# Performance work log

Measured on AMD Instinct MI355X. Metric: run time of the kernel, lower is better.

Reference implementation:

```python
import jax, jax.numpy as jnp
import numpy as np

THRESHOLD = 0.004  # graph_threshold from init_kwargs
EPS = 1e-12


def setup_inputs() -> dict:
    key = jax.random.key(0)
    kf, kw = jax.random.split(key)
    features = jax.random.normal(kf, (8192, 128), dtype=jnp.float32)
    weight = jax.random.normal(kw, (128, 128), dtype=jnp.float32)
    return {"features": features, "weight": weight}


def reference(features, weight):
    # Pairwise state fidelity: squared dot product of row-normalized vectors.
    n = features.shape[0]
    xn = features / (jnp.linalg.norm(features, axis=1, keepdims=True) + EPS)
    fid = (xn @ xn.T) ** 2  # [N, N]
    # Edge weight 1.0 where fid >= threshold (secondary=None); no self-loops.
    adj = (fid >= THRESHOLD).astype(features.dtype)
    adj = adj * (1.0 - jnp.eye(n, dtype=features.dtype))
    aggregated = adj @ features  # [N, F]
    # relu(W @ agg.T).T == relu(agg @ W.T)
    return jax.nn.relu(aggregated @ weight.T)
```

## Files before the change

### kernel.cpp

```cpp
#include <hip/hip_runtime.h>
#include <math.h>

#define NROWS 8192
#define NF    128
#define THRF  0.004f
#define BM    128
#define BN    64
#define QN    2048
#define NITER 32

typedef _Float16 f16;
typedef __attribute__((ext_vector_type(8))) _Float16 f16x8;
typedef __attribute__((ext_vector_type(4))) float f32x4;

#define MFMA16F(a, b, c) __builtin_amdgcn_mfma_f32_16x16x32_f16(a, b, c, 0, 0, 0)

#define RH_OFF 0
#define RL_OFF 32768
#define TB_OFF 65536
#define PB_OFF 98304
#define IJ_OFF 114688
#define SM_BYTES 115200

typedef __attribute__((address_space(1))) const unsigned int g_u32;
typedef __attribute__((address_space(3))) unsigned int l_u32;

__device__ __forceinline__ void gload16(const void* g, void* l) {
    __builtin_amdgcn_global_load_lds((g_u32*)g, (l_u32*)l, 16, 0, 0);
}

__device__ __forceinline__ unsigned short f16bits(f16 x) {
    return __builtin_bit_cast(unsigned short, x);
}

__global__ __launch_bounds__(256) void zero_k(float* __restrict__ out) {
    int idx = blockIdx.x * 512 + threadIdx.x;
    f32x4 z = {0.f, 0.f, 0.f, 0.f};
    reinterpret_cast<f32x4*>(out)[idx]       = z;
    reinterpret_cast<f32x4*>(out)[idx + 256] = z;
}

__global__ __launch_bounds__(256) void prep_k(const float* __restrict__ X,
                                              float* __restrict__ inv_norm,
                                              unsigned short* __restrict__ Xh,
                                              unsigned short* __restrict__ Xl,
                                              unsigned short* __restrict__ XhT) {
    __shared__ unsigned short sT[64][136];
    const int t  = threadIdx.x;
    const int jb = blockIdx.x * 64;
    const int row = t >> 2, c0 = (t & 3) * 32;
    const int grow = jb + row;

    float v[32];
    {
        const float* src = X + (size_t)grow * NF + c0;
        #pragma unroll
        for (int k = 0; k < 8; ++k) {
            f32x4 e = *reinterpret_cast<const f32x4*>(src + 4 * k);
            v[4 * k]     = e[0]; v[4 * k + 1] = e[1];
            v[4 * k + 2] = e[2]; v[4 * k + 3] = e[3];
        }
    }
    float ss = 0.f;
    #pragma unroll
    for (int k = 0; k < 32; ++k) ss += v[k] * v[k];
    ss += __shfl_xor(ss, 1);
    ss += __shfl_xor(ss, 2);
    if ((t & 3) == 0) inv_norm[grow] = 1.0f / (sqrtf(ss) + 1e-12f);

    #pragma unroll
    for (int k = 0; k < 4; ++k) {
        unsigned hw[4], lw[4];
        #pragma unroll
        for (int p = 0; p < 4; ++p) {
            float a = v[8 * k + 2 * p], b = v[8 * k + 2 * p + 1];
            f16 ha = (f16)a, hb = (f16)b;
            f16 la = (f16)((a - (float)ha) * 2048.0f);
            f16 lb = (f16)((b - (float)hb) * 2048.0f);
            hw[p] = (unsigned)f16bits(ha) | ((unsigned)f16bits(hb) << 16);
            lw[p] = (unsigned)f16bits(la) | ((unsigned)f16bits(lb) << 16);
        }
        uint4 h4 = {hw[0], hw[1], hw[2], hw[3]};
        uint4 l4 = {lw[0], lw[1], lw[2], lw[3]};
        *reinterpret_cast<uint4*>(Xh + (size_t)grow * NF + c0 + 8 * k) = h4;
        *reinterpret_cast<uint4*>(Xl + (size_t)grow * NF + c0 + 8 * k) = l4;
        unsigned* sp = reinterpret_cast<unsigned*>(&sT[row][c0 + 8 * k]);
        sp[0] = hw[0]; sp[1] = hw[1]; sp[2] = hw[2]; sp[3] = hw[3];
    }
    __syncthreads();
    {
        int f = t >> 1, qh = t & 1;
        unsigned um[16];
        #pragma unroll
        for (int m = 0; m < 16; ++m) {
            int j = 32 * qh + 2 * m;
            um[m] = (unsigned)sT[j][f] | ((unsigned)sT[j + 1][f] << 16);
        }
        unsigned* dst = reinterpret_cast<unsigned*>(XhT + (size_t)f * NROWS + jb + 32 * qh);
        #pragma unroll
        for (int m = 0; m < 16; ++m) dst[m] = um[m];
    }
}

__device__ __forceinline__ void issue_tiles(const unsigned short* __restrict__ Xh,
                                            const unsigned short* __restrict__ Xl,
                                            const unsigned short* __restrict__ XhT,
                                            char* SM, int w, int l, int jwin, int buf) {
    const int r16 = l >> 4, c16 = l & 15;
    #pragma unroll
    for (int u = 0; u < 2; ++u) {
        int jloc = 8 * w + 4 * u + r16;
        size_t src = (size_t)(jwin + jloc) * NF + ((c16 ^ (jloc & 15)) << 3);
        gload16(Xh + src, SM + RH_OFF + buf * 16384 + (8 * w + 4 * u) * 256);
        gload16(Xl + src, SM + RL_OFF + buf * 16384 + (8 * w + 4 * u) * 256);
    }
    const int r8 = l >> 3, c8 = l & 7;
    #pragma unroll
    for (int u = 0; u < 2; ++u) {
        int floc = 16 * w + 8 * u + r8;
        const unsigned short* src = XhT + (size_t)floc * NROWS + jwin + ((c8 ^ (floc & 7)) << 3);
        gload16(src, SM + TB_OFF + buf * 16384 + (16 * w + 8 * u) * 128);
    }
}

__global__ __launch_bounds__(512, 2) void fused_k(const unsigned short* __restrict__ Xh,
                                                  const unsigned short* __restrict__ Xl,
                                                  const unsigned short* __restrict__ XhT,
                                                  const float* __restrict__ inv_norm,
                                                  float* __restrict__ out) {
    __shared__ __align__(16) char SM[SM_BYTES];
    const int t = threadIdx.x;
    const int w = t >> 6, l = t & 63, l15 = l & 15, h = l >> 4;
    const int im2 = w >> 1;
    const int jn2 = w & 1;
    const int bid   = blockIdx.x;
    const int ibase = (bid >> 2) * BM;
    const int qbase = (bid & 3) * QN;

    f16x8 aH[2][4], aL[2][4];
    #pragma unroll
    for (int is = 0; is < 2; ++is) {
        const size_t ro = (size_t)(ibase + 32 * im2 + 16 * is + l15) * NF;
        #pragma unroll
        for (int ks = 0; ks < 4; ++ks) {
            aH[is][ks] = *reinterpret_cast<const f16x8*>(Xh + ro + 32 * ks + 8 * h);
            aL[is][ks] = *reinterpret_cast<const f16x8*>(Xl + ro + 32 * ks + 8 * h);
        }
    }
    float invI2[8];
    #pragma unroll
    for (int is = 0; is < 2; ++is)
        #pragma unroll
        for (int q = 0; q < 4; ++q) {
            float x = inv_norm[ibase + 32 * im2 + 16 * is + 4 * h + q];
            invI2[is * 4 + q] = x * x;
        }

    issue_tiles(Xh, Xl, XhT, SM, w, l, qbase, 0);
    if (t < BN) { float x = inv_norm[qbase + t]; ((float*)(SM + IJ_OFF))[t] = x * x; }

    f32x4 agg[2][4];
    #pragma unroll
    for (int is = 0; is < 2; ++is)
        #pragma unroll
        for (int fs = 0; fs < 4; ++fs)
            #pragma unroll
            for (int q = 0; q < 4; ++q) agg[is][fs][q] = 0.f;

    for (int it = 0; it < NITER; ++it) {
        const int buf  = it & 1;
        const int jwin = qbase + it * BN;
        __syncthreads();
        if (it + 1 < NITER) {
            issue_tiles(Xh, Xl, XhT, SM, w, l, jwin + BN, buf ^ 1);
            if (t < BN) {
                float x = inv_norm[jwin + BN + t];
                ((float*)(SM + IJ_OFF))[(buf ^ 1) * BN + t] = x * x;
            }
        }
        const char* rh = SM + RH_OFF + buf * 16384;
        const char* rl = SM + RL_OFF + buf * 16384;
        f32x4 Shi[2][2], Slo[2][2];
        #pragma unroll
        for (int js = 0; js < 2; ++js)
            #pragma unroll
            for (int is = 0; is < 2; ++is)
                #pragma unroll
                for (int q = 0; q < 4; ++q) { Shi[js][is][q] = 0.f; Slo[js][is][q] = 0.f; }
        __builtin_amdgcn_s_setprio(1);
        #pragma unroll
        for (int ks = 0; ks < 4; ++ks) {
            #pragma unroll
            for (int js = 0; js < 2; ++js) {
                int jl = 32 * jn2 + 16 * js + l15;
                int boff = jl * 256 + (((4 * ks + h) ^ (jl & 15)) << 4);
                f16x8 bh = *reinterpret_cast<const f16x8*>(rh + boff);
                f16x8 bl = *reinterpret_cast<const f16x8*>(rl + boff);
                #pragma unroll
                for (int is = 0; is < 2; ++is) {
                    Shi[js][is] = MFMA16F(aH[is][ks], bh, Shi[js][is]);
                    Slo[js][is] = MFMA16F(aL[is][ks], bh, Slo[js][is]);
                    Slo[js][is] = MFMA16F(aH[is][ks], bl, Slo[js][is]);
                }
            }
        }
        __builtin_amdgcn_s_setprio(0);

        #pragma unroll
        for (int js = 0; js < 2; ++js) {
            int jc = 32 * jn2 + 16 * js + l15;
            float ij2 = ((const float*)(SM + IJ_OFF))[buf * BN + jc];
            #pragma unroll
            for (int is = 0; is < 2; ++is) {
                int di = (jwin + jc) - (ibase + 32 * im2 + 16 * is + 4 * h);
                #pragma unroll
                for (int q = 0; q < 4; ++q) {
                    float vv = Shi[js][is][q] + Slo[js][is][q] * (1.0f / 2048.0f);
                    float t2 = vv * vv * invI2[is * 4 + q] * ij2;
                    bool p = (t2 >= THRF) && (di != q);
                    int il = 32 * im2 + 16 * is + 4 * h + q;
                    int pb = il * 128 + ((jc * 2) ^ ((il & 7) << 4));
                    *reinterpret_cast<unsigned short*>(SM + PB_OFF + pb) =
                        p ? (unsigned short)0x3C00 : (unsigned short)0;
                }
            }
        }
        asm volatile("s_waitcnt lgkmcnt(0)\n\ts_barrier" ::: "memory");

        const char* tbp = SM + TB_OFF + buf * 16384;
        __builtin_amdgcn_s_setprio(1);
        #pragma unroll
        for (int kj = 0; kj < 2; ++kj) {
            f16x8 pa[2];
            #pragma unroll
            for (int is = 0; is < 2; ++is) {
                int ir = 32 * im2 + 16 * is + l15;
                pa[is] = *reinterpret_cast<const f16x8*>(
                    SM + PB_OFF + ir * 128 + ((64 * kj + 16 * h) ^ ((ir & 7) << 4)));
            }
            #pragma unroll
            for (int fs = 0; fs < 4; ++fs) {
                int f = 64 * jn2 + 16 * fs + l15;
                f16x8 bt = *reinterpret_cast<const f16x8*>(
                    tbp + f * 128 + ((64 * kj + 16 * h) ^ ((f & 7) << 4)));
                agg[0][fs] = MFMA16F(pa[0], bt, agg[0][fs]);
                agg[1][fs] = MFMA16F(pa[1], bt, agg[1][fs]);
            }
        }
        __builtin_amdgcn_s_setprio(0);
    }

    #pragma unroll
    for (int is = 0; is < 2; ++is)
        #pragma unroll
        for (int fs = 0; fs < 4; ++fs) {
            int col = 64 * jn2 + 16 * fs + l15;
            #pragma unroll
            for (int q = 0; q < 4; ++q) {
                int row = ibase + 32 * im2 + 16 * is + 4 * h + q;
                atomicAdd(&out[(size_t)row * NF + col], agg[is][fs][q]);
            }
        }
}

__global__ __launch_bounds__(256) void combine_k(const float* __restrict__ Wm,
                                                 float* __restrict__ out) {
    __shared__ float sW[NF * NF];
    __shared__ float sSum[32][132];
    const int t = threadIdx.x;
    const size_t base = (size_t)blockIdx.x * 32 * NF;
    #pragma unroll
    for (int k = 0; k < 16; ++k) {
        int u4 = t + 256 * k;
        reinterpret_cast<f32x4*>(sW)[u4] = reinterpret_cast<const f32x4*>(Wm)[u4];
    }
    #pragma unroll
    for (int k = 0; k < 4; ++k) {
        int u4 = t + 256 * k;
        f32x4 v = reinterpret_cast<const f32x4*>(out + base)[u4];
        *reinterpret_cast<f32x4*>(&sSum[u4 >> 5][(4 * u4) & 127]) = v;
    }
    __syncthreads();
    const int r = t & 31, og = t >> 5;
    float acc[16];
    #pragma unroll
    for (int oi = 0; oi < 16; ++oi) acc[oi] = 0.f;
    #pragma unroll 8
    for (int k4 = 0; k4 < 32; ++k4) {
        f32x4 a4 = *reinterpret_cast<const f32x4*>(&sSum[r][4 * k4]);
        #pragma unroll
        for (int oi = 0; oi < 16; ++oi) {
            f32x4 w4 = *reinterpret_cast<const f32x4*>(&sW[(og * 16 + oi) * NF + 4 * k4]);
            acc[oi] += a4[0] * w4[0] + a4[1] * w4[1] + a4[2] * w4[2] + a4[3] * w4[3];
        }
    }
    #pragma unroll
    for (int o4 = 0; o4 < 4; ++o4) {
        f32x4 v4;
        #pragma unroll
        for (int e = 0; e < 4; ++e) {
            float v = acc[o4 * 4 + e];
            v4[e] = v > 0.f ? v : 0.f;
        }
        *reinterpret_cast<f32x4*>(out + base + r * NF + og * 16 + o4 * 4) = v4;
    }
}

extern "C" void kernel_launch(void* const* d_in, const int* in_sizes, int n_in,
                              void* d_out, int out_size, void* d_ws, size_t ws_size,
                              hipStream_t stream) {
    const float* feat = (const float*)d_in[0];
    const float* Wm   = (const float*)d_in[1];
    float* out        = (float*)d_out;

    char* ws = (char*)d_ws;
    unsigned short* Xh  = (unsigned short*)(ws);
    unsigned short* Xl  = (unsigned short*)(ws + (2u << 20));
    unsigned short* XhT = (unsigned short*)(ws + (4u << 20));
    float* inv_norm     = (float*)(ws + (6u << 20));

    zero_k<<<NROWS * NF / 2048, 256, 0, stream>>>(out);
    prep_k<<<NROWS / 64, 256, 0, stream>>>(feat, inv_norm, Xh, Xl, XhT);
    fused_k<<<256, 512, 0, stream>>>(Xh, Xl, XhT, inv_norm, out);
    combine_k<<<NROWS / 32, 256, 0, stream>>>(Wm, out);
}
```

Before: 107.6 us.

## Split fused kernel into dedicated producer and consumer wavefronts

Adds four producer wavefronts per block (768 threads) that issue all global-to-LDS tile loads and inverse-norm staging, while the original eight wavefronts only run the MFMA fidelity and aggregation stages. This takes load-issue work off the compute waves so prefetch overlaps compute more cleanly. The cost is extra threads per block, a launch bound change that may restrict registers per thread, and producers that sit idle at every barrier. Each block still needs about 115 KB of LDS, so the requested three blocks per CU likely cannot co-reside.

```diff
diff --git a/kernel.cpp b/kernel.cpp
--- a/kernel.cpp
+++ b/kernel.cpp
@@ -102,28 +102,28 @@
     }
 }
 
-__device__ __forceinline__ void issue_tiles(const unsigned short* __restrict__ Xh,
-                                            const unsigned short* __restrict__ Xl,
-                                            const unsigned short* __restrict__ XhT,
-                                            char* SM, int w, int l, int jwin, int buf) {
+__device__ __forceinline__ void issue_tiles_p(const unsigned short* __restrict__ Xh,
+                                              const unsigned short* __restrict__ Xl,
+                                              const unsigned short* __restrict__ XhT,
+                                              char* SM, int p, int l, int jwin, int buf) {
     const int r16 = l >> 4, c16 = l & 15;
     #pragma unroll
-    for (int u = 0; u < 2; ++u) {
-        int jloc = 8 * w + 4 * u + r16;
+    for (int u = 0; u < 4; ++u) {
+        int jloc = 16 * p + 4 * u + r16;
         size_t src = (size_t)(jwin + jloc) * NF + ((c16 ^ (jloc & 15)) << 3);
-        gload16(Xh + src, SM + RH_OFF + buf * 16384 + (8 * w + 4 * u) * 256);
-        gload16(Xl + src, SM + RL_OFF + buf * 16384 + (8 * w + 4 * u) * 256);
+        gload16(Xh + src, SM + RH_OFF + buf * 16384 + (16 * p + 4 * u) * 256);
+        gload16(Xl + src, SM + RL_OFF + buf * 16384 + (16 * p + 4 * u) * 256);
     }
     const int r8 = l >> 3, c8 = l & 7;
     #pragma unroll
-    for (int u = 0; u < 2; ++u) {
-        int floc = 16 * w + 8 * u + r8;
+    for (int u = 0; u < 4; ++u) {
+        int floc = 32 * p + 8 * u + r8;
         const unsigned short* src = XhT + (size_t)floc * NROWS + jwin + ((c8 ^ (floc & 7)) << 3);
-        gload16(src, SM + TB_OFF + buf * 16384 + (16 * w + 8 * u) * 128);
-    }
-}
-
-__global__ __launch_bounds__(512, 2) void fused_k(const unsigned short* __restrict__ Xh,
+        gload16(src, SM + TB_OFF + buf * 16384 + (32 * p + 8 * u) * 128);
+    }
+}
+
+__global__ __launch_bounds__(768, 3) void fused_k(const unsigned short* __restrict__ Xh,
                                                   const unsigned short* __restrict__ Xl,
                                                   const unsigned short* __restrict__ XhT,
                                                   const float* __restrict__ inv_norm,
@@ -131,33 +131,46 @@
     __shared__ __align__(16) char SM[SM_BYTES];
     const int t = threadIdx.x;
     const int w = t >> 6, l = t & 63, l15 = l & 15, h = l >> 4;
-    const int im2 = w >> 1;
+    const bool producer = (w >= 8);
+    const int im2 = (w >> 1) & 3;
     const int jn2 = w & 1;
     const int bid   = blockIdx.x;
     const int ibase = (bid >> 2) * BM;
     const int qbase = (bid & 3) * QN;
 
     f16x8 aH[2][4], aL[2][4];
-    #pragma unroll
-    for (int is = 0; is < 2; ++is) {
-        const size_t ro = (size_t)(ibase + 32 * im2 + 16 * is + l15) * NF;
-        #pragma unroll
-        for (int ks = 0; ks < 4; ++ks) {
-            aH[is][ks] = *reinterpret_cast<const f16x8*>(Xh + ro + 32 * ks + 8 * h);
-            aL[is][ks] = *reinterpret_cast<const f16x8*>(Xl + ro + 32 * ks + 8 * h);
-        }
-    }
     float invI2[8];
-    #pragma unroll
-    for (int is = 0; is < 2; ++is)
-        #pragma unroll
-        for (int q = 0; q < 4; ++q) {
-            float x = inv_norm[ibase + 32 * im2 + 16 * is + 4 * h + q];
-            invI2[is * 4 + q] = x * x;
-        }
-
-    issue_tiles(Xh, Xl, XhT, SM, w, l, qbase, 0);
-    if (t < BN) { float x = inv_norm[qbase + t]; ((float*)(SM + IJ_OFF))[t] = x * x; }
+    if (!producer) {
+        #pragma unroll
+        for (int is = 0; is < 2; ++is) {
+            const size_t ro = (size_t)(ibase + 32 * im2 + 16 * is + l15) * NF;
+            #pragma unroll
+            for (int ks = 0; ks < 4; ++ks) {
+                aH[is][ks] = *reinterpret_cast<const f16x8*>(Xh + ro + 32 * ks + 8 * h);
+                aL[is][ks] = *reinterpret_cast<const f16x8*>(Xl + ro + 32 * ks + 8 * h);
+            }
+        }
+        #pragma unroll
+        for (int is = 0; is < 2; ++is)
+            #pragma unroll
+            for (int ks = 0; ks < 4; ++ks) {
+                asm volatile("" : "+v"(aH[is][ks]));
+                asm volatile("" : "+v"(aL[is][ks]));
+            }
+        #pragma unroll
+        for (int is = 0; is < 2; ++is)
+            #pragma unroll
+            for (int q = 0; q < 4; ++q) {
+                float x = inv_norm[ibase + 32 * im2 + 16 * is + 4 * h + q];
+                invI2[is * 4 + q] = x * x;
+            }
+    } else {
+        issue_tiles_p(Xh, Xl, XhT, SM, w - 8, l, qbase, 0);
+        if (w == 8) {
+            float x = inv_norm[qbase + l];
+            ((float*)(SM + IJ_OFF))[l] = x * x;
+        }
+    }
 
     f32x4 agg[2][4];
     #pragma unroll
@@ -171,96 +184,103 @@
         const int buf  = it & 1;
         const int jwin = qbase + it * BN;
         __syncthreads();
-        if (it + 1 < NITER) {
-            issue_tiles(Xh, Xl, XhT, SM, w, l, jwin + BN, buf ^ 1);
-            if (t < BN) {
-                float x = inv_norm[jwin + BN + t];
-                ((float*)(SM + IJ_OFF))[(buf ^ 1) * BN + t] = x * x;
-            }
-        }
-        const char* rh = SM + RH_OFF + buf * 16384;
-        const char* rl = SM + RL_OFF + buf * 16384;
-        f32x4 Shi[2][2], Slo[2][2];
-        #pragma unroll
-        for (int js = 0; js < 2; ++js)
-            #pragma unroll
-            for (int is = 0; is < 2; ++is)
-                #pragma unroll
-                for (int q = 0; q < 4; ++q) { Shi[js][is][q] = 0.f; Slo[js][is][q] = 0.f; }
-        __builtin_amdgcn_s_setprio(1);
-        #pragma unroll
-        for (int ks = 0; ks < 4; ++ks) {
+        if (producer) {
+            if (it + 1 < NITER) {
+                issue_tiles_p(Xh, Xl, XhT, SM, w - 8, l, jwin + BN, buf ^ 1);
+                if (w == 8) {
+                    float x = inv_norm[jwin + BN + l];
+                    ((float*)(SM + IJ_OFF))[(buf ^ 1) * BN + l] = x * x;
+                }
+            }
+        } else {
+            const char* rh = SM + RH_OFF + buf * 16384;
+            const char* rl = SM + RL_OFF + buf * 16384;
+            f32x4 Shi[2][2], Slo[2][2];
+            #pragma unroll
+            for (int js = 0; js < 2; ++js)
+                #pragma unroll
+                for (int is = 0; is < 2; ++is)
+                    #pragma unroll
+                    for (int q = 0; q < 4; ++q) { Shi[js][is][q] = 0.f; Slo[js][is][q] = 0.f; }
+            __builtin_amdgcn_s_setprio(1);
+            #pragma unroll
+            for (int ks = 0; ks < 4; ++ks) {
+                #pragma unroll
+                for (int js = 0; js < 2; ++js) {
+                    int jl = 32 * jn2 + 16 * js + l15;
+                    int boff = jl * 256 + (((4 * ks + h) ^ (jl & 15)) << 4);
+                    f16x8 bh = *reinterpret_cast<const f16x8*>(rh + boff);
+                    f16x8 bl = *reinterpret_cast<const f16x8*>(rl + boff);
+                    #pragma unroll
+                    for (int is = 0; is < 2; ++is) {
+                        Shi[js][is] = MFMA16F(aH[is][ks], bh, Shi[js][is]);
+                        Slo[js][is] = MFMA16F(aL[is][ks], bh, Slo[js][is]);
+                        Slo[js][is] = MFMA16F(aH[is][ks], bl, Slo[js][is]);
+                    }
+                }
+            }
+            __builtin_amdgcn_s_setprio(0);
+
             #pragma unroll
             for (int js = 0; js < 2; ++js) {
-                int jl = 32 * jn2 + 16 * js + l15;
-                int boff = jl * 256 + (((4 * ks + h) ^ (jl & 15)) << 4);
-                f16x8 bh = *reinterpret_cast<const f16x8*>(rh + boff);
-                f16x8 bl = *reinterpret_cast<const f16x8*>(rl + boff);
+                int jc = 32 * jn2 + 16 * js + l15;
+                float ij2 = ((const float*)(SM + IJ_OFF))[buf * BN + jc];
                 #pragma unroll
                 for (int is = 0; is < 2; ++is) {
-                    Shi[js][is] = MFMA16F(aH[is][ks], bh, Shi[js][is]);
-                    Slo[js][is] = MFMA16F(aL[is][ks], bh, Slo[js][is]);
-                    Slo[js][is] = MFMA16F(aH[is][ks], bl, Slo[js][is]);
-                }
-            }
-        }
-        __builtin_amdgcn_s_setprio(0);
-
-        #pragma unroll
-        for (int js = 0; js < 2; ++js) {
-            int jc = 32 * jn2 + 16 * js + l15;
-            float ij2 = ((const float*)(SM + IJ_OFF))[buf * BN + jc];
-            #pragma unroll
-            for (int is = 0; is < 2; ++is) {
-                int di = (jwin + jc) - (ibase + 32 * im2 + 16 * is + 4 * h);
+                    int di = (jwin + jc) - (ibase + 32 * im2 + 16 * is + 4 * h);
+                    #pragma unroll
+                    for (int q = 0; q < 4; ++q) {
+                        float vv = Shi[js][is][q] + Slo[js][is][q] * (1.0f / 2048.0f);
+                        float t2 = vv * vv * invI2[is * 4 + q] * ij2;
+                        bool p = (t2 >= THRF) && (di != q);
+                        int il = 32 * im2 + 16 * is + 4 * h + q;
+                        int pb = il * 128 + ((jc * 2) ^ ((il & 7) << 4));
+                        *reinterpret_cast<unsigned short*>(SM + PB_OFF + pb) =
+                            p ? (unsigned short)0x3C00 : (unsigned short)0;
+                    }
+                }
+            }
+        }
+        asm volatile("s_waitcnt lgkmcnt(0)\n\ts_barrier" ::: "memory");
+
+        if (!producer) {
+            const char* tbp = SM + TB_OFF + buf * 16384;
+            __builtin_amdgcn_s_setprio(1);
+            #pragma unroll
+            for (int kj = 0; kj < 2; ++kj) {
+                f16x8 pa[2];
+                #pragma unroll
+                for (int is = 0; is < 2; ++is) {
+                    int ir = 32 * im2 + 16 * is + l15;
+                    pa[is] = *reinterpret_cast<const f16x8*>(
+                        SM + PB_OFF + ir * 128 + ((64 * kj + 16 * h) ^ ((ir & 7) << 4)));
+                }
+                #pragma unroll
+                for (int fs = 0; fs < 4; ++fs) {
+                    int f = 64 * jn2 + 16 * fs + l15;
+                    f16x8 bt = *reinterpret_cast<const f16x8*>(
+                        tbp + f * 128 + ((64 * kj + 16 * h) ^ ((f & 7) << 4)));
+                    agg[0][fs] = MFMA16F(pa[0], bt, agg[0][fs]);
+                    agg[1][fs] = MFMA16F(pa[1], bt, agg[1][fs]);
+                }
+            }
+            __builtin_amdgcn_s_setprio(0);
+        }
+    }
+
+    if (!producer) {
+        #pragma unroll
+        for (int is = 0; is < 2; ++is)
+            #pragma unroll
+            for (int fs = 0; fs < 4; ++fs) {
+                int col = 64 * jn2 + 16 * fs + l15;
                 #pragma unroll
                 for (int q = 0; q < 4; ++q) {
-                    float vv = Shi[js][is][q] + Slo[js][is][q] * (1.0f / 2048.0f);
-                    float t2 = vv * vv * invI2[is * 4 + q] * ij2;
-                    bool p = (t2 >= THRF) && (di != q);
-                    int il = 32 * im2 + 16 * is + 4 * h + q;
-                    int pb = il * 128 + ((jc * 2) ^ ((il & 7) << 4));
-                    *reinterpret_cast<unsigned short*>(SM + PB_OFF + pb) =
-                        p ? (unsigned short)0x3C00 : (unsigned short)0;
-                }
-            }
-        }
-        asm volatile("s_waitcnt lgkmcnt(0)\n\ts_barrier" ::: "memory");
-
-        const char* tbp = SM + TB_OFF + buf * 16384;
-        __builtin_amdgcn_s_setprio(1);
-        #pragma unroll
-        for (int kj = 0; kj < 2; ++kj) {
-            f16x8 pa[2];
-            #pragma unroll
-            for (int is = 0; is < 2; ++is) {
-                int ir = 32 * im2 + 16 * is + l15;
-                pa[is] = *reinterpret_cast<const f16x8*>(
-                    SM + PB_OFF + ir * 128 + ((64 * kj + 16 * h) ^ ((ir & 7) << 4)));
-            }
-            #pragma unroll
-            for (int fs = 0; fs < 4; ++fs) {
-                int f = 64 * jn2 + 16 * fs + l15;
-                f16x8 bt = *reinterpret_cast<const f16x8*>(
-                    tbp + f * 128 + ((64 * kj + 16 * h) ^ ((f & 7) << 4)));
-                agg[0][fs] = MFMA16F(pa[0], bt, agg[0][fs]);
-                agg[1][fs] = MFMA16F(pa[1], bt, agg[1][fs]);
-            }
-        }
-        __builtin_amdgcn_s_setprio(0);
-    }
-
-    #pragma unroll
-    for (int is = 0; is < 2; ++is)
-        #pragma unroll
-        for (int fs = 0; fs < 4; ++fs) {
-            int col = 64 * jn2 + 16 * fs + l15;
-            #pragma unroll
-            for (int q = 0; q < 4; ++q) {
-                int row = ibase + 32 * im2 + 16 * is + 4 * h + q;
-                atomicAdd(&out[(size_t)row * NF + col], agg[is][fs][q]);
-            }
-        }
+                    int row = ibase + 32 * im2 + 16 * is + 4 * h + q;
+                    atomicAdd(&out[(size_t)row * NF + col], agg[is][fs][q]);
+                }
+            }
+    }
 }
 
 __global__ __launch_bounds__(256) void combine_k(const float* __restrict__ Wm,
@@ -321,6 +341,6 @@
 
     zero_k<<<NROWS * NF / 2048, 256, 0, stream>>>(out);
     prep_k<<<NROWS / 64, 256, 0, stream>>>(feat, inv_norm, Xh, Xl, XhT);
-    fused_k<<<256, 512, 0, stream>>>(Xh, Xl, XhT, inv_norm, out);
+    fused_k<<<256, 768, 0, stream>>>(Xh, Xl, XhT, inv_norm, out);
     combine_k<<<NROWS / 32, 256, 0, stream>>>(Wm, out);
 }
```

New measurement: 192.9 us. +79.2%, slower.
